# Optimization experiments

Measured on AMD Instinct MI355X. Metric: run time of the kernel, lower is better.

The kernel has to match this reference:

```python
import jax, jax.numpy as jnp
import numpy as np
import math

B, L = 4, 900
D_MODEL, D_STATE, D_INNER, DT_RANK = 256, 16, 512, 16


def setup_inputs() -> dict:
    key = jax.random.key(0)
    ks = jax.random.split(key, 10)
    nrm = lambda k, shape, s: jax.random.normal(k, shape, jnp.float32) * s
    hidden_states = jax.random.normal(ks[0], (B, L, D_MODEL), jnp.float32)
    W_in = nrm(ks[1], (2 * D_INNER, D_MODEL), D_MODEL ** -0.5)
    W_xproj = nrm(ks[2], (DT_RANK + 2 * D_STATE, D_INNER), D_INNER ** -0.5)
    s = DT_RANK ** -0.5
    W_dt = jax.random.uniform(ks[3], (D_INNER, DT_RANK), jnp.float32, -s, s)
    # dt bias init: inv_softplus of dt ~ LogUniform[1e-3, 0.1]
    dt = jnp.exp(jax.random.uniform(ks[4], (D_INNER,), jnp.float32)
                 * (math.log(0.1) - math.log(1e-3)) + math.log(1e-3))
    b_dt = dt + jnp.log(-jnp.expm1(-dt))
    A_log = jnp.broadcast_to(jnp.log(jnp.arange(1, D_STATE + 1, dtype=jnp.float32)),
                             (D_INNER, D_STATE))
    W_global = nrm(ks[5], (2 * D_INNER, 2 * D_INNER), (2 * D_INNER) ** -0.5)
    W_gate = nrm(ks[6], (2 * D_INNER, 2 * D_INNER), (2 * D_INNER) ** -0.5)
    W_out = nrm(ks[7], (D_MODEL, 2 * D_INNER), (2 * D_INNER) ** -0.5)
    return {
        'hidden_states': hidden_states, 'W_in': W_in, 'W_xproj': W_xproj,
        'W_dt': W_dt, 'b_dt': b_dt,
        'A_log_f': jnp.array(A_log), 'A_log_b': jnp.array(A_log),
        'D_f': jnp.ones(D_INNER, jnp.float32), 'D_b': jnp.ones(D_INNER, jnp.float32),
        'W_global': W_global, 'b_global': jnp.zeros(2 * D_INNER, jnp.float32),
        'W_gate': W_gate, 'b_gate': jnp.zeros(2 * D_INNER, jnp.float32),
        'W_out': W_out,
    }


def _selective_scan(u, delta, A, Bm, Cm, D):
    """u, delta: (b,l,d); Bm, Cm: (b,l,n); A: (d,n); D: (d,). Returns (b,l,d)."""
    dA = jnp.exp(jnp.einsum('bld,dn->lbdn', delta, A))          # discretized A
    dBu = jnp.einsum('bld,bln->lbdn', delta * u, Bm)             # dt*B*u
    Ct = jnp.transpose(Cm, (1, 0, 2))                            # (l,b,n)

    def step(h, inp):
        dA_t, dBu_t, c = inp
        h = dA_t * h + dBu_t                                     # (b,d,n)
        return h, jnp.einsum('bdn,bn->bd', h, c)

    h0 = jnp.zeros((u.shape[0], u.shape[2], A.shape[1]), u.dtype)
    _, ys = jax.lax.scan(step, h0, (dA, dBu, Ct))
    return jnp.transpose(ys, (1, 0, 2)) + D * u                  # D skip connection


def reference(hidden_states, W_in, W_xproj, W_dt, b_dt, A_log_f, A_log_b,
              D_f, D_b, W_global, b_global, W_gate, b_gate, W_out):
    silu = lambda t: t * jax.nn.sigmoid(t)
    xz = hidden_states @ W_in.T                                  # (b,l,2*di)
    x, z = jnp.split(xz, 2, axis=-1)
    x = silu(x)
    x_dbl = x @ W_xproj.T                                        # (b,l,r+2n)
    dt_r = x_dbl[..., :DT_RANK]
    Bm = x_dbl[..., DT_RANK:DT_RANK + D_STATE]
    Cm = x_dbl[..., DT_RANK + D_STATE:]
    dt = jax.nn.softplus(dt_r @ W_dt.T + b_dt)                   # (b,l,di)

    A_f = -jnp.exp(A_log_f)
    A_b = -jnp.exp(A_log_b)
    flip = lambda t: t[:, ::-1]
    y_f = _selective_scan(x, dt, A_f, Bm, Cm, D_f)
    y_b = flip(_selective_scan(flip(x), flip(dt), A_b, flip(Bm), flip(Cm), D_b))
    zg = silu(z)
    y = jnp.concatenate([y_f * zg, y_b * zg], axis=-1)           # (b,l,2*di)
    # global gate: pooled features -> global_proj -> y_gate_proj -> sigmoid
    g = jax.nn.sigmoid((y.mean(axis=1) @ W_global.T + b_global) @ W_gate.T + b_gate)
    y = y * g[:, None, :]
    return y @ W_out.T                                           # (b,l,d_model)
```

## Files before the change

### kernel.cpp

```cpp
#include <hip/hip_runtime.h>
#include <hip/hip_bf16.h>

#define BB 4
#define LL 900
#define DMODEL 256
#define DSTATE 16
#define DINNER 512
#define DTRANK 16
#define BL (BB*LL)
#define NC 75
#define LC 12

typedef __bf16 bf16x8 __attribute__((ext_vector_type(8)));
typedef __bf16 bf16x4 __attribute__((ext_vector_type(4)));
typedef float f32x4 __attribute__((ext_vector_type(4)));

__device__ __forceinline__ float silu_f(float v) { return v / (1.f + __expf(-v)); }

#define N_HID  (BL*DMODEL)
#define N_WIN  (2*DINNER*DMODEL)
#define N_WXP  (48*DINNER)
#define N_WOUT (DMODEL*2*DINNER)
#define N_TOT  (N_HID+N_WIN+N_WXP+N_WOUT)
__global__ void cvt_inputs(const float* __restrict__ hidden, const float* __restrict__ Win,
                           const float* __restrict__ Wxp, const float* __restrict__ Wout,
                           __bf16* __restrict__ hh, __bf16* __restrict__ wih,
                           __bf16* __restrict__ wxh, __bf16* __restrict__ woh)
{
    int idx = blockIdx.x * 256 + threadIdx.x;
    if (idx >= N_TOT) return;
    const float* src; __bf16* dst; int off;
    if (idx < N_HID)                        { src = hidden; dst = hh;  off = idx; }
    else if (idx < N_HID+N_WIN)             { src = Win;    dst = wih; off = idx - N_HID; }
    else if (idx < N_HID+N_WIN+N_WXP)       { src = Wxp;    dst = wxh; off = idx - N_HID - N_WIN; }
    else                                    { src = Wout;   dst = woh; off = idx - N_HID - N_WIN - N_WXP; }
    dst[off] = (__bf16)src[off];
}

__launch_bounds__(256)
__global__ void gemm_silu(const __bf16* __restrict__ A, const __bf16* __restrict__ B,
                          __bf16* __restrict__ xb, __bf16* __restrict__ zb)
{
    constexpr int WM = 3, WN = 2, K = 256, nk = K >> 5;
    constexpr int M = BL, N = 2 * DINNER;
    int wave = (blockIdx.x * 256 + threadIdx.x) >> 6;
    int ntN = N / (16 * WN);
    if (wave >= (M / (16 * WM)) * ntN) return;
    int tm = wave / ntN, tn = wave % ntN;
    int lane = threadIdx.x & 63, q = lane >> 4, r = lane & 15;

    const bf16x8* Ar[WM]; const bf16x8* Br[WN];
    #pragma unroll
    for (int mi = 0; mi < WM; ++mi)
        Ar[mi] = (const bf16x8*)(A + (size_t)(tm * 48 + mi * 16 + r) * K);
    #pragma unroll
    for (int ni = 0; ni < WN; ++ni)
        Br[ni] = (const bf16x8*)(B + (size_t)(tn * 32 + ni * 16 + r) * K);
    f32x4 acc[WM][WN];
    #pragma unroll
    for (int mi = 0; mi < WM; ++mi)
        #pragma unroll
        for (int ni = 0; ni < WN; ++ni) acc[mi][ni] = (f32x4){0.f,0.f,0.f,0.f};

    #pragma unroll
    for (int kk = 0; kk < nk; ++kk) {
        int idx = kk * 4 + q;
        bf16x8 av[WM], bv[WN];
        #pragma unroll
        for (int mi = 0; mi < WM; ++mi) av[mi] = Ar[mi][idx];
        #pragma unroll
        for (int ni = 0; ni < WN; ++ni) bv[ni] = Br[ni][idx];
        #pragma unroll
        for (int mi = 0; mi < WM; ++mi)
            #pragma unroll
            for (int ni = 0; ni < WN; ++ni)
                acc[mi][ni] = __builtin_amdgcn_mfma_f32_16x16x32_bf16(av[mi], bv[ni], acc[mi][ni], 0, 0, 0);
    }
    #pragma unroll
    for (int mi = 0; mi < WM; ++mi)
        #pragma unroll
        for (int ni = 0; ni < WN; ++ni) {
            int col = tn * 32 + ni * 16 + r;
            #pragma unroll
            for (int i = 0; i < 4; ++i) {
                int row = tm * 48 + mi * 16 + q * 4 + i;
                float s = silu_f(acc[mi][ni][i]);
                if (col < DINNER) xb[(size_t)row * DINNER + col] = (__bf16)s;
                else              zb[(size_t)row * DINNER + (col - DINNER)] = (__bf16)s;
            }
        }
}

__launch_bounds__(256)
__global__ void gemm2_dt(const __bf16* __restrict__ A, const __bf16* __restrict__ B,
                         const float* __restrict__ Wdt, const float* __restrict__ bdt,
                         float* __restrict__ dtBC, float* __restrict__ dtb)
{
    constexpr int WN = 3, K = 512, KSL = 128, nk = KSL >> 5;
    __shared__ float lds[4][16 * 48];
    int tm = blockIdx.x;
    int wv = threadIdx.x >> 6, kOff = wv * KSL;
    int lane = threadIdx.x & 63, q = lane >> 4, r = lane & 15;

    const bf16x8* Ar = (const bf16x8*)(A + (size_t)(tm * 16 + r) * K + kOff);
    const bf16x8* Br[WN];
    #pragma unroll
    for (int ni = 0; ni < WN; ++ni)
        Br[ni] = (const bf16x8*)(B + (size_t)(ni * 16 + r) * K + kOff);
    f32x4 acc[WN];
    #pragma unroll
    for (int ni = 0; ni < WN; ++ni) acc[ni] = (f32x4){0.f,0.f,0.f,0.f};

    #pragma unroll
    for (int kk = 0; kk < nk; ++kk) {
        int idx = kk * 4 + q;
        bf16x8 av = Ar[idx];
        #pragma unroll
        for (int ni = 0; ni < WN; ++ni)
            acc[ni] = __builtin_amdgcn_mfma_f32_16x16x32_bf16(av, Br[ni][idx], acc[ni], 0, 0, 0);
    }
    #pragma unroll
    for (int ni = 0; ni < WN; ++ni) {
        int col = ni * 16 + r;
        #pragma unroll
        for (int i = 0; i < 4; ++i)
            lds[wv][(q * 4 + i) * 48 + col] = acc[ni][i];
    }
    __syncthreads();
    for (int e = threadIdx.x; e < 16 * 48; e += 256) {
        float s = lds[0][e] + lds[1][e] + lds[2][e] + lds[3][e];
        lds[0][e] = s;
        int row = e / 48, col = e % 48;
        dtBC[(size_t)(tm * 16 + row) * 48 + col] = s;
    }
    __syncthreads();
    for (int it = 0; it < 32; ++it) {
        int e = threadIdx.x + it * 256;
        int row = e >> 9, d = e & 511;
        const float* wr = Wdt + (size_t)d * DTRANK;
        float s = bdt[d];
        #pragma unroll
        for (int k = 0; k < DTRANK; ++k) s = fmaf(lds[0][row * 48 + k], wr[k], s);
        dtb[(size_t)(tm * 16 + row) * DINNER + d] = (s > 15.f) ? s : __logf(1.f + __expf(s));
    }
}

__global__ void scan_pass1(const float* __restrict__ dtb,
                           const __bf16* __restrict__ xb,
                           const float* __restrict__ dtBC,
                           const float* __restrict__ AlogF, const float* __restrict__ AlogB,
                           float* __restrict__ Pbuf, float* __restrict__ Qbuf)
{
    int b = blockIdx.z, dir = blockIdx.y;
    int c = blockIdx.x >> 2, dgrp = blockIdx.x & 3;
    int d = dgrp * 128 + threadIdx.x;
    const float* Alog = dir ? AlogB : AlogF;
    float a2[DSTATE];
    #pragma unroll
    for (int n = 0; n < DSTATE; ++n) a2[n] = -__expf(Alog[d * DSTATE + n]) * 1.44269504f;
    float h[DSTATE];
    #pragma unroll
    for (int n = 0; n < DSTATE; ++n) h[n] = 0.f;
    float sdt = 0.f;

    #pragma unroll 4
    for (int il = 0; il < LC; ++il) {
        int i = c * LC + il;
        int l = dir ? (LL - 1 - i) : i;
        size_t base = (size_t)b * LL + l;
        float dtv = dtb[base * DINNER + d];
        float u = (float)xb[base * DINNER + d];
        float du = dtv * u;
        const f32x4* Bp = (const f32x4*)(dtBC + base * 48 + DTRANK);
        f32x4 Bq[4];
        #pragma unroll
        for (int j = 0; j < 4; ++j) Bq[j] = Bp[j];
        sdt += dtv;
        #pragma unroll
        for (int n = 0; n < DSTATE; ++n)
            h[n] = fmaf(exp2f(dtv * a2[n]), h[n], du * Bq[n >> 2][n & 3]);
    }
    size_t o = (((size_t)(b * 2 + dir) * NC + c) * DSTATE) * DINNER + d;
    #pragma unroll
    for (int n = 0; n < DSTATE; ++n) {
        Pbuf[o + (size_t)n * DINNER] = exp2f(sdt * a2[n]);
        Qbuf[o + (size_t)n * DINNER] = h[n];
    }
}

__global__ void scan_stitch(float* __restrict__ Pbuf, const float* __restrict__ Qbuf)
{
    int idx = blockIdx.x * 256 + threadIdx.x;
    int bd = idx >> 13;
    int rem = idx & 8191;
    size_t base = (size_t)bd * NC * 8192 + rem;
    float H = 0.f;
    for (int cb = 0; cb < NC; cb += 15) {
        float Pv[15], Qv[15];
        #pragma unroll
        for (int j = 0; j < 15; ++j) {
            size_t o = base + (size_t)(cb + j) * 8192;
            Pv[j] = Pbuf[o];
            Qv[j] = Qbuf[o];
        }
        #pragma unroll
        for (int j = 0; j < 15; ++j) {
            Pbuf[base + (size_t)(cb + j) * 8192] = H;
            H = fmaf(Pv[j], H, Qv[j]);
        }
    }
}

__global__ void scan_pass3(const float* __restrict__ dtb,
                           const __bf16* __restrict__ xb,
                           const float* __restrict__ dtBC,
                           const float* __restrict__ AlogF, const float* __restrict__ AlogB,
                           const float* __restrict__ Df, const float* __restrict__ Db,
                           const __bf16* __restrict__ zb,
                           const float* __restrict__ H0buf,
                           __bf16* __restrict__ yb,
                           float* __restrict__ partial)
{
    int b = blockIdx.z, dir = blockIdx.y;
    int c = blockIdx.x >> 2, dgrp = blockIdx.x & 3;
    int d = dgrp * 128 + threadIdx.x;
    const float* Alog = dir ? AlogB : AlogF;
    float a2[DSTATE];
    #pragma unroll
    for (int n = 0; n < DSTATE; ++n) a2[n] = -__expf(Alog[d * DSTATE + n]) * 1.44269504f;
    float Dd = dir ? Db[d] : Df[d];
    size_t o = (((size_t)(b * 2 + dir) * NC + c) * DSTATE) * DINNER + d;
    float h[DSTATE];
    #pragma unroll
    for (int n = 0; n < DSTATE; ++n) h[n] = H0buf[o + (size_t)n * DINNER];
    float ysum = 0.f;

    #pragma unroll 4
    for (int il = 0; il < LC; ++il) {
        int i = c * LC + il;
        int l = dir ? (LL - 1 - i) : i;
        size_t base = (size_t)b * LL + l;
        float dtv = dtb[base * DINNER + d];
        float u = (float)xb[base * DINNER + d];
        float du = dtv * u;
        const f32x4* Bp = (const f32x4*)(dtBC + base * 48 + DTRANK);
        f32x4 Bq[4], Cq[4];
        #pragma unroll
        for (int j = 0; j < 4; ++j) Bq[j] = Bp[j];
        #pragma unroll
        for (int j = 0; j < 4; ++j) Cq[j] = Bp[4 + j];
        float p = 0.f;
        #pragma unroll
        for (int n = 0; n < DSTATE; ++n) {
            h[n] = fmaf(exp2f(dtv * a2[n]), h[n], du * Bq[n >> 2][n & 3]);
            p = fmaf(h[n], Cq[n >> 2][n & 3], p);
        }
        float zg = (float)zb[base * DINNER + d];
        float yv = (p + Dd * u) * zg;
        size_t yo = base * (2 * DINNER) + dir * DINNER + d;
        yb[yo] = (__bf16)yv;
        ysum += yv;
    }
    partial[((size_t)b * NC + c) * 1024 + dir * DINNER + d] = ysum;
}

__global__ void mean2(const float* __restrict__ partial, float* __restrict__ ymean)
{
    int i = blockIdx.x * 256 + threadIdx.x;
    int b = i >> 10, ch = i & 1023;
    float s = 0.f;
    #pragma unroll 5
    for (int c = 0; c < NC; ++c) s += partial[((size_t)b * NC + c) * 1024 + ch];
    ymean[i] = s / (float)LL;
}

template<int SIG>
__global__ void gemv1024(const float* __restrict__ vin,
                         const float* __restrict__ W,
                         const float* __restrict__ bias,
                         float* __restrict__ vout)
{
    int wv = (blockIdx.x * blockDim.x + threadIdx.x) >> 6;
    int b = wv >> 10, j = wv & 1023;
    int lane = threadIdx.x & 63;
    const float* wr = W + (size_t)j * 1024;
    const float* vr = vin + (size_t)b * 1024;
    float s = 0.f;
    for (int k = lane; k < 1024; k += 64) s = fmaf(vr[k], wr[k], s);
    #pragma unroll
    for (int o = 32; o; o >>= 1) s += __shfl_xor(s, o);
    if (lane == 0) {
        s += bias[j];
        vout[wv] = SIG ? (1.f / (1.f + __expf(-s))) : s;
    }
}

__global__ void scale_y(__bf16* __restrict__ yb, const float* __restrict__ g)
{
    int idx = blockIdx.x * 256 + threadIdx.x;
    int e = idx * 8;
    int ch = e & 1023;
    int b = (e >> 10) / LL;
    bf16x8 v = reinterpret_cast<bf16x8*>(yb)[idx];
    const f32x4* gp = (const f32x4*)(g + b * 1024 + ch);
    f32x4 g0 = gp[0], g1 = gp[1];
    #pragma unroll
    for (int j = 0; j < 4; ++j) v[j] = (__bf16)((float)v[j] * g0[j]);
    #pragma unroll
    for (int j = 0; j < 4; ++j) v[4 + j] = (__bf16)((float)v[4 + j] * g1[j]);
    reinterpret_cast<bf16x8*>(yb)[idx] = v;
}

__launch_bounds__(256)
__global__ void gemm8_comb(const __bf16* __restrict__ A, const __bf16* __restrict__ B,
                           float* __restrict__ out)
{
    constexpr int WM = 3, WN = 2, K = 1024, KSL = 512, nk = KSL >> 5;
    constexpr int N = DMODEL, ntN = N / (16 * WN);
    __shared__ float lds[2][2][48 * 32];
    int wv = threadIdx.x >> 6;
    int tLoc = wv >> 1, ks = wv & 1;
    int tIdx = blockIdx.x * 2 + tLoc;
    int tm = tIdx / ntN, tn = tIdx % ntN;
    int kOff = ks * KSL;
    int lane = threadIdx.x & 63, q = lane >> 4, r = lane & 15;

    const bf16x8* Ar[WM]; const bf16x8* Br[WN];
    #pragma unroll
    for (int mi = 0; mi < WM; ++mi)
        Ar[mi] = (const bf16x8*)(A + (size_t)(tm * 48 + mi * 16 + r) * K + kOff);
    #pragma unroll
    for (int ni = 0; ni < WN; ++ni)
        Br[ni] = (const bf16x8*)(B + (size_t)(tn * 32 + ni * 16 + r) * K + kOff);
    f32x4 acc[WM][WN];
    #pragma unroll
    for (int mi = 0; mi < WM; ++mi)
        #pragma unroll
        for (int ni = 0; ni < WN; ++ni) acc[mi][ni] = (f32x4){0.f,0.f,0.f,0.f};

    #pragma unroll
    for (int kk = 0; kk < nk; ++kk) {
        int idx = kk * 4 + q;
        bf16x8 av[WM], bv[WN];
        #pragma unroll
        for (int mi = 0; mi < WM; ++mi) av[mi] = Ar[mi][idx];
        #pragma unroll
        for (int ni = 0; ni < WN; ++ni) bv[ni] = Br[ni][idx];
        #pragma unroll
        for (int mi = 0; mi < WM; ++mi)
            #pragma unroll
            for (int ni = 0; ni < WN; ++ni)
                acc[mi][ni] = __builtin_amdgcn_mfma_f32_16x16x32_bf16(av[mi], bv[ni], acc[mi][ni], 0, 0, 0);
    }
    #pragma unroll
    for (int mi = 0; mi < WM; ++mi)
        #pragma unroll
        for (int ni = 0; ni < WN; ++ni) {
            int col = ni * 16 + r;
            #pragma unroll
            for (int i = 0; i < 4; ++i)
                lds[tLoc][ks][(mi * 16 + q * 4 + i) * 32 + col] = acc[mi][ni][i];
        }
    __syncthreads();
    for (int e = threadIdx.x; e < 2 * 1536; e += 256) {
        int tl = (e >= 1536) ? 1 : 0;
        int idx = e - tl * 1536;
        int row = idx >> 5, col = idx & 31;
        int tg = blockIdx.x * 2 + tl;
        int gm = (tg / ntN) * 48 + row, gn = (tg % ntN) * 32 + col;
        out[(size_t)gm * N + gn] = lds[tl][0][idx] + lds[tl][1][idx];
    }
}

extern "C" void kernel_launch(void* const* d_in, const int* in_sizes, int n_in,
                              void* d_out, int out_size, void* d_ws, size_t ws_size,
                              hipStream_t stream)
{
    const float* hidden  = (const float*)d_in[0];
    const float* W_in    = (const float*)d_in[1];
    const float* W_xproj = (const float*)d_in[2];
    const float* W_dt    = (const float*)d_in[3];
    const float* b_dt    = (const float*)d_in[4];
    const float* A_log_f = (const float*)d_in[5];
    const float* A_log_b = (const float*)d_in[6];
    const float* D_f     = (const float*)d_in[7];
    const float* D_b     = (const float*)d_in[8];
    const float* W_glob  = (const float*)d_in[9];
    const float* b_glob  = (const float*)d_in[10];
    const float* W_gate  = (const float*)d_in[11];
    const float* b_gate  = (const float*)d_in[12];
    const float* W_out   = (const float*)d_in[13];
    float* out = (float*)d_out;

    char* w = (char*)d_ws;
    __bf16* xb    = (__bf16*)w; w += (size_t)BL * DINNER * 2;
    __bf16* zb    = (__bf16*)w; w += (size_t)BL * DINNER * 2;
    float* dtBC   = (float*)w;  w += (size_t)BL * 48 * 4;
    float* dtb    = (float*)w;  w += (size_t)BL * DINNER * 4;
    __bf16* yb    = (__bf16*)w; w += (size_t)BL * 2 * DINNER * 2;
    float* partial= (float*)w;  w += (size_t)BB * NC * 1024 * 4;
    float* ymean  = (float*)w;  w += (size_t)BB * 1024 * 4;
    float* t1     = (float*)w;  w += (size_t)BB * 1024 * 4;
    float* gbuf   = (float*)w;  w += (size_t)BB * 1024 * 4;
    __bf16* hh    = (__bf16*)w; w += (size_t)N_HID * 2;
    __bf16* wih   = (__bf16*)w; w += (size_t)N_WIN * 2;
    __bf16* wxh   = (__bf16*)w; w += (size_t)N_WXP * 2;
    __bf16* woh   = (__bf16*)w; w += (size_t)N_WOUT * 2;
    float* Pbuf   = (float*)w;  w += (size_t)BB * 2 * NC * DSTATE * DINNER * 4;
    float* Qbuf   = (float*)w;  w += (size_t)BB * 2 * NC * DSTATE * DINNER * 4;

    cvt_inputs<<<dim3((N_TOT + 255) / 256), dim3(256), 0, stream>>>(
        hidden, W_in, W_xproj, W_out, hh, wih, wxh, woh);
    gemm_silu<<<dim3(600), dim3(256), 0, stream>>>(hh, wih, xb, zb);
    gemm2_dt<<<dim3(225), dim3(256), 0, stream>>>(xb, wxh, W_dt, b_dt, dtBC, dtb);
    scan_pass1<<<dim3(NC * 4, 2, BB), dim3(128), 0, stream>>>(
        dtb, xb, dtBC, A_log_f, A_log_b, Pbuf, Qbuf);
    scan_stitch<<<dim3(256), dim3(256), 0, stream>>>(Pbuf, Qbuf);
    scan_pass3<<<dim3(NC * 4, 2, BB), dim3(128), 0, stream>>>(
        dtb, xb, dtBC, A_log_f, A_log_b, D_f, D_b, zb, Pbuf, yb, partial);
    mean2<<<dim3(16), dim3(256), 0, stream>>>(partial, ymean);
    gemv1024<0><<<dim3(1024), dim3(256), 0, stream>>>(ymean, W_glob, b_glob, t1);
    gemv1024<1><<<dim3(1024), dim3(256), 0, stream>>>(t1, W_gate, b_gate, gbuf);
    scale_y<<<dim3(BL * 1024 / 8 / 256), dim3(256), 0, stream>>>(yb, gbuf);
    gemm8_comb<<<dim3(300), dim3(256), 0, stream>>>(yb, woh, out);
}
```

Measured before the change: 223.0 us.

## Store dt, chunk states and gate weights in bf16; recompute chunk decay

The softplus dt tensor is stored as bf16 instead of fp32. The per-chunk scan carry now stores only the chunk dt sum, with the decay factor recomputed via exp2 in the stitch kernel. The chunk states and stitched initial states are held in bf16. The global and gate GEMV weights are also converted to bf16 in the input-conversion kernel. The goal is to cut the large Pbuf/Qbuf and dtb traffic through the scan passes, at the cost of reduced precision in the recurrent carried state and extra conversion work for the 1024x1024 weights.

```diff
diff --git a/kernel.cpp b/kernel.cpp
--- a/kernel.cpp
+++ b/kernel.cpp
@@ -21,19 +21,24 @@
 #define N_WIN  (2*DINNER*DMODEL)
 #define N_WXP  (48*DINNER)
 #define N_WOUT (DMODEL*2*DINNER)
-#define N_TOT  (N_HID+N_WIN+N_WXP+N_WOUT)
+#define N_WG   (2*DINNER*2*DINNER)
+#define N_TOT  (N_HID+N_WIN+N_WXP+N_WOUT+2*N_WG)
 __global__ void cvt_inputs(const float* __restrict__ hidden, const float* __restrict__ Win,
                            const float* __restrict__ Wxp, const float* __restrict__ Wout,
+                           const float* __restrict__ Wglob, const float* __restrict__ Wgate,
                            __bf16* __restrict__ hh, __bf16* __restrict__ wih,
-                           __bf16* __restrict__ wxh, __bf16* __restrict__ woh)
+                           __bf16* __restrict__ wxh, __bf16* __restrict__ woh,
+                           __bf16* __restrict__ wgb, __bf16* __restrict__ wtb)
 {
     int idx = blockIdx.x * 256 + threadIdx.x;
     if (idx >= N_TOT) return;
     const float* src; __bf16* dst; int off;
-    if (idx < N_HID)                        { src = hidden; dst = hh;  off = idx; }
-    else if (idx < N_HID+N_WIN)             { src = Win;    dst = wih; off = idx - N_HID; }
-    else if (idx < N_HID+N_WIN+N_WXP)       { src = Wxp;    dst = wxh; off = idx - N_HID - N_WIN; }
-    else                                    { src = Wout;   dst = woh; off = idx - N_HID - N_WIN - N_WXP; }
+    if (idx < N_HID)                              { src = hidden; dst = hh;  off = idx; }
+    else if (idx < N_HID+N_WIN)                   { src = Win;    dst = wih; off = idx - N_HID; }
+    else if (idx < N_HID+N_WIN+N_WXP)             { src = Wxp;    dst = wxh; off = idx - N_HID - N_WIN; }
+    else if (idx < N_HID+N_WIN+N_WXP+N_WOUT)      { src = Wout;   dst = woh; off = idx - N_HID - N_WIN - N_WXP; }
+    else if (idx < N_HID+N_WIN+N_WXP+N_WOUT+N_WG) { src = Wglob;  dst = wgb; off = idx - N_HID - N_WIN - N_WXP - N_WOUT; }
+    else                                          { src = Wgate;  dst = wtb; off = idx - N_HID - N_WIN - N_WXP - N_WOUT - N_WG; }
     dst[off] = (__bf16)src[off];
 }
 
@@ -94,7 +99,7 @@
 __launch_bounds__(256)
 __global__ void gemm2_dt(const __bf16* __restrict__ A, const __bf16* __restrict__ B,
                          const float* __restrict__ Wdt, const float* __restrict__ bdt,
-                         float* __restrict__ dtBC, float* __restrict__ dtb)
+                         float* __restrict__ dtBC, __bf16* __restrict__ dtb)
 {
     constexpr int WN = 3, K = 512, KSL = 128, nk = KSL >> 5;
     __shared__ float lds[4][16 * 48];
@@ -141,15 +146,16 @@
         float s = bdt[d];
         #pragma unroll
         for (int k = 0; k < DTRANK; ++k) s = fmaf(lds[0][row * 48 + k], wr[k], s);
-        dtb[(size_t)(tm * 16 + row) * DINNER + d] = (s > 15.f) ? s : __logf(1.f + __expf(s));
-    }
-}
-
-__global__ void scan_pass1(const float* __restrict__ dtb,
+        float dtv = (s > 15.f) ? s : __logf(1.f + __expf(s));
+        dtb[(size_t)(tm * 16 + row) * DINNER + d] = (__bf16)dtv;
+    }
+}
+
+__global__ void scan_pass1(const __bf16* __restrict__ dtb,
                            const __bf16* __restrict__ xb,
                            const float* __restrict__ dtBC,
                            const float* __restrict__ AlogF, const float* __restrict__ AlogB,
-                           float* __restrict__ Pbuf, float* __restrict__ Qbuf)
+                           float* __restrict__ sdtBuf, __bf16* __restrict__ Qbuf)
 {
     int b = blockIdx.z, dir = blockIdx.y;
     int c = blockIdx.x >> 2, dgrp = blockIdx.x & 3;
@@ -168,7 +174,7 @@
         int i = c * LC + il;
         int l = dir ? (LL - 1 - i) : i;
         size_t base = (size_t)b * LL + l;
-        float dtv = dtb[base * DINNER + d];
+        float dtv = (float)dtb[base * DINNER + d];
         float u = (float)xb[base * DINNER + d];
         float du = dtv * u;
         const f32x4* Bp = (const f32x4*)(dtBC + base * 48 + DTRANK);
@@ -180,44 +186,49 @@
         for (int n = 0; n < DSTATE; ++n)
             h[n] = fmaf(exp2f(dtv * a2[n]), h[n], du * Bq[n >> 2][n & 3]);
     }
-    size_t o = (((size_t)(b * 2 + dir) * NC + c) * DSTATE) * DINNER + d;
-    #pragma unroll
-    for (int n = 0; n < DSTATE; ++n) {
-        Pbuf[o + (size_t)n * DINNER] = exp2f(sdt * a2[n]);
-        Qbuf[o + (size_t)n * DINNER] = h[n];
-    }
-}
-
-__global__ void scan_stitch(float* __restrict__ Pbuf, const float* __restrict__ Qbuf)
+    int bd = b * 2 + dir;
+    sdtBuf[((size_t)bd * NC + c) * DINNER + d] = sdt;
+    size_t o = (((size_t)bd * NC + c) * DSTATE) * DINNER + d;
+    #pragma unroll
+    for (int n = 0; n < DSTATE; ++n)
+        Qbuf[o + (size_t)n * DINNER] = (__bf16)h[n];
+}
+
+__global__ void scan_stitch(const float* __restrict__ sdtBuf,
+                            const float* __restrict__ AlogF, const float* __restrict__ AlogB,
+                            __bf16* __restrict__ Qbuf)
 {
     int idx = blockIdx.x * 256 + threadIdx.x;
     int bd = idx >> 13;
     int rem = idx & 8191;
-    size_t base = (size_t)bd * NC * 8192 + rem;
+    int n = rem >> 9, d = rem & 511;
+    const float* Alog = (bd & 1) ? AlogB : AlogF;
+    float a2 = -__expf(Alog[d * DSTATE + n]) * 1.44269504f;
+    size_t qbase = (size_t)bd * NC * 8192 + rem;
+    size_t sbase = (size_t)bd * NC * DINNER + d;
     float H = 0.f;
     for (int cb = 0; cb < NC; cb += 15) {
-        float Pv[15], Qv[15];
+        float Qv[15], Sv[15];
         #pragma unroll
         for (int j = 0; j < 15; ++j) {
-            size_t o = base + (size_t)(cb + j) * 8192;
-            Pv[j] = Pbuf[o];
-            Qv[j] = Qbuf[o];
+            Qv[j] = (float)Qbuf[qbase + (size_t)(cb + j) * 8192];
+            Sv[j] = sdtBuf[sbase + (size_t)(cb + j) * DINNER];
         }
         #pragma unroll
         for (int j = 0; j < 15; ++j) {
-            Pbuf[base + (size_t)(cb + j) * 8192] = H;
-            H = fmaf(Pv[j], H, Qv[j]);
+            Qbuf[qbase + (size_t)(cb + j) * 8192] = (__bf16)H;
+            H = fmaf(exp2f(Sv[j] * a2), H, Qv[j]);
         }
     }
 }
 
-__global__ void scan_pass3(const float* __restrict__ dtb,
+__global__ void scan_pass3(const __bf16* __restrict__ dtb,
                            const __bf16* __restrict__ xb,
                            const float* __restrict__ dtBC,
                            const float* __restrict__ AlogF, const float* __restrict__ AlogB,
                            const float* __restrict__ Df, const float* __restrict__ Db,
                            const __bf16* __restrict__ zb,
-                           const float* __restrict__ H0buf,
+                           const __bf16* __restrict__ H0buf,
                            __bf16* __restrict__ yb,
                            float* __restrict__ partial)
 {
@@ -232,7 +243,7 @@
     size_t o = (((size_t)(b * 2 + dir) * NC + c) * DSTATE) * DINNER + d;
     float h[DSTATE];
     #pragma unroll
-    for (int n = 0; n < DSTATE; ++n) h[n] = H0buf[o + (size_t)n * DINNER];
+    for (int n = 0; n < DSTATE; ++n) h[n] = (float)H0buf[o + (size_t)n * DINNER];
     float ysum = 0.f;
 
     #pragma unroll 4
@@ -240,7 +251,7 @@
         int i = c * LC + il;
         int l = dir ? (LL - 1 - i) : i;
         size_t base = (size_t)b * LL + l;
-        float dtv = dtb[base * DINNER + d];
+        float dtv = (float)dtb[base * DINNER + d];
         float u = (float)xb[base * DINNER + d];
         float du = dtv * u;
         const f32x4* Bp = (const f32x4*)(dtBC + base * 48 + DTRANK);
@@ -276,17 +287,17 @@
 
 template<int SIG>
 __global__ void gemv1024(const float* __restrict__ vin,
-                         const float* __restrict__ W,
+                         const __bf16* __restrict__ W,
                          const float* __restrict__ bias,
                          float* __restrict__ vout)
 {
     int wv = (blockIdx.x * blockDim.x + threadIdx.x) >> 6;
     int b = wv >> 10, j = wv & 1023;
     int lane = threadIdx.x & 63;
-    const float* wr = W + (size_t)j * 1024;
+    const __bf16* wr = W + (size_t)j * 1024;
     const float* vr = vin + (size_t)b * 1024;
     float s = 0.f;
-    for (int k = lane; k < 1024; k += 64) s = fmaf(vr[k], wr[k], s);
+    for (int k = lane; k < 1024; k += 64) s = fmaf(vr[k], (float)wr[k], s);
     #pragma unroll
     for (int o = 32; o; o >>= 1) s += __shfl_xor(s, o);
     if (lane == 0) {
@@ -396,7 +407,7 @@
     __bf16* xb    = (__bf16*)w; w += (size_t)BL * DINNER * 2;
     __bf16* zb    = (__bf16*)w; w += (size_t)BL * DINNER * 2;
     float* dtBC   = (float*)w;  w += (size_t)BL * 48 * 4;
-    float* dtb    = (float*)w;  w += (size_t)BL * DINNER * 4;
+    __bf16* dtb   = (__bf16*)w; w += (size_t)BL * DINNER * 2;
     __bf16* yb    = (__bf16*)w; w += (size_t)BL * 2 * DINNER * 2;
     float* partial= (float*)w;  w += (size_t)BB * NC * 1024 * 4;
     float* ymean  = (float*)w;  w += (size_t)BB * 1024 * 4;
@@ -406,21 +417,23 @@
     __bf16* wih   = (__bf16*)w; w += (size_t)N_WIN * 2;
     __bf16* wxh   = (__bf16*)w; w += (size_t)N_WXP * 2;
     __bf16* woh   = (__bf16*)w; w += (size_t)N_WOUT * 2;
-    float* Pbuf   = (float*)w;  w += (size_t)BB * 2 * NC * DSTATE * DINNER * 4;
-    float* Qbuf   = (float*)w;  w += (size_t)BB * 2 * NC * DSTATE * DINNER * 4;
+    __bf16* wgb   = (__bf16*)w; w += (size_t)N_WG * 2;
+    __bf16* wtb   = (__bf16*)w; w += (size_t)N_WG * 2;
+    float* sdtBuf = (float*)w;  w += (size_t)BB * 2 * NC * DINNER * 4;
+    __bf16* Qbuf  = (__bf16*)w; w += (size_t)BB * 2 * NC * DSTATE * DINNER * 2;
 
     cvt_inputs<<<dim3((N_TOT + 255) / 256), dim3(256), 0, stream>>>(
-        hidden, W_in, W_xproj, W_out, hh, wih, wxh, woh);
+        hidden, W_in, W_xproj, W_out, W_glob, W_gate, hh, wih, wxh, woh, wgb, wtb);
     gemm_silu<<<dim3(600), dim3(256), 0, stream>>>(hh, wih, xb, zb);
     gemm2_dt<<<dim3(225), dim3(256), 0, stream>>>(xb, wxh, W_dt, b_dt, dtBC, dtb);
     scan_pass1<<<dim3(NC * 4, 2, BB), dim3(128), 0, stream>>>(
-        dtb, xb, dtBC, A_log_f, A_log_b, Pbuf, Qbuf);
-    scan_stitch<<<dim3(256), dim3(256), 0, stream>>>(Pbuf, Qbuf);
+        dtb, xb, dtBC, A_log_f, A_log_b, sdtBuf, Qbuf);
+    scan_stitch<<<dim3(256), dim3(256), 0, stream>>>(sdtBuf, A_log_f, A_log_b, Qbuf);
     scan_pass3<<<dim3(NC * 4, 2, BB), dim3(128), 0, stream>>>(
-        dtb, xb, dtBC, A_log_f, A_log_b, D_f, D_b, zb, Pbuf, yb, partial);
+        dtb, xb, dtBC, A_log_f, A_log_b, D_f, D_b, zb, Qbuf, yb, partial);
     mean2<<<dim3(16), dim3(256), 0, stream>>>(partial, ymean);
-    gemv1024<0><<<dim3(1024), dim3(256), 0, stream>>>(ymean, W_glob, b_glob, t1);
-    gemv1024<1><<<dim3(1024), dim3(256), 0, stream>>>(t1, W_gate, b_gate, gbuf);
+    gemv1024<0><<<dim3(1024), dim3(256), 0, stream>>>(ymean, wgb, b_glob, t1);
+    gemv1024<1><<<dim3(1024), dim3(256), 0, stream>>>(t1, wtb, b_gate, gbuf);
     scale_y<<<dim3(BL * 1024 / 8 / 256), dim3(256), 0, stream>>>(yb, gbuf);
     gemm8_comb<<<dim3(300), dim3(256), 0, stream>>>(yb, woh, out);
 }
```

After: 219.7 us. No clear change (-1.5%).
